# Kernel optimization log

Measured on AMD Instinct MI355X. Metric: run time of the kernel, lower is better.

Reference implementation:

```python
import jax, jax.numpy as jnp
import numpy as np

E = 8
DIMS = [512, 1024, 1024, 512]
BATCH = 2048


def _init_w(key, shape):
    a = np.sqrt(6.0 / (shape[-2] * shape[-1]))
    return jax.random.uniform(key, shape, dtype=jnp.float32, minval=-a, maxval=a)


def setup_inputs() -> dict:
    key = jax.random.key(0)
    ks = jax.random.split(key, 8)
    inp = {
        "weight_blend": jax.random.uniform(ks[0], (BATCH, E), dtype=jnp.float32),
        "x": jax.random.normal(ks[1], (BATCH, DIMS[0]), dtype=jnp.float32),
    }
    for i in range(3):
        inp[f"W{i}"] = _init_w(ks[2 + i], (E, DIMS[i + 1], DIMS[i]))
        inp[f"B{i}"] = jnp.zeros((E, DIMS[i + 1], 1), dtype=jnp.float32)
    return inp


def reference(weight_blend, x, W0, B0, W1, B1, W2, B2):
    Ws = [W0, W1, W2]
    Bs = [B0, B1, B2]
    acts = [jax.nn.elu, jax.nn.elu, None]
    for W, B, act in zip(Ws, Bs, acts):
        # dropout p=0 -> identity
        # blended-expert GEMM: sum_e wb[b,e] * (W[e] @ x[b]) == einsum
        t = jnp.einsum("be,eoi,bi->bo", weight_blend, W, x)
        bias = jnp.einsum("be,eo->bo", weight_blend, B[..., 0])
        x = t + bias
        if act is not None:
            x = act(x)
    return x
```

## Files before the change

### kernel.cpp

```cpp
#include <hip/hip_runtime.h>
#include <math.h>

typedef __attribute__((ext_vector_type(8))) short bf16x8;
typedef __attribute__((ext_vector_type(4))) float f32x4;

#define NEXP 8
#define BATCH 2048

__device__ __forceinline__ unsigned short f2bf(float f) {
    union { float f; unsigned u; } v; v.f = f;
    unsigned r = v.u + 0x7FFFu + ((v.u >> 16) & 1u);
    return (unsigned short)(r >> 16);
}

__device__ __forceinline__ float elu_fast(float v) {
    return v > 0.f ? v : (exp2f(v * 1.4426950408889634f) - 1.0f);
}

__global__ __launch_bounds__(256) void pack_all(
    const float* __restrict__ W0, const float* __restrict__ W1,
    const float* __restrict__ W2, const float* __restrict__ x,
    unsigned short* __restrict__ W0p, unsigned short* __restrict__ W1p,
    unsigned short* __restrict__ W2p, unsigned short* __restrict__ x0p)
{
    __shared__ float T[128 * 36];
    const int bid = blockIdx.x, t = threadIdx.x;

    if (bid < 10240) {
        const float* W; unsigned short* out; int KB, Din, Dout, U, lin;
        if (bid < 2048)      { W = W0; out = W0p; KB = 16; Din = 512;  Dout = 1024; U = 4; lin = bid; }
        else if (bid < 6144) { W = W1; out = W1p; KB = 32; Din = 1024; Dout = 1024; U = 4; lin = bid - 2048; }
        else                 { W = W2; out = W2p; KB = 32; Din = 1024; Dout = 512;  U = 2; lin = bid - 6144; }
        const int e  = lin & 7;
        const int r  = lin >> 3;
        const int kb = r % KB;
        const int nb = r / KB;
        const int N0 = nb * 16 * U;
        const int K0 = kb * 32;
        for (int it = 0; it < U / 2; ++it) {
            const int idx = t + 256 * it;
            const int nl = idx >> 3, k4 = (idx & 7) * 4;
            float4 v = *(const float4*)(W + ((size_t)e * Dout + N0 + nl) * Din + K0 + k4);
            *(float4*)(T + nl * 36 + k4) = v;
        }
        __syncthreads();
        if (t < 64 * U) {
            const int u = t >> 6, l = t & 63;
            const float* p = T + (u * 16 + (l & 15)) * 36 + (l >> 4) * 8;
            bf16x8 h;
            #pragma unroll
            for (int j = 0; j < 8; ++j) h[j] = (short)f2bf(p[j]);
            *(bf16x8*)(out + (size_t)lin * (U * 512) + t * 8) = h;
        }
    } else {
        const int lin = bid - 10240;
        const int kb = lin & 15, mb = lin >> 4;
        for (int it = 0; it < 4; ++it) {
            const int idx = t + 256 * it;
            const int ml = idx >> 3, k4 = (idx & 7) * 4;
            float4 v = *(const float4*)(x + (size_t)(mb * 128 + ml) * 512 + kb * 32 + k4);
            *(float4*)(T + ml * 36 + k4) = v;
        }
        __syncthreads();
        #pragma unroll
        for (int it = 0; it < 2; ++it) {
            const int s = t + 256 * it;
            const int g = s >> 6, l = s & 63;
            const float* p = T + (g * 16 + (l & 15)) * 36 + (l >> 4) * 8;
            bf16x8 h;
            #pragma unroll
            for (int j = 0; j < 8; ++j) h[j] = (short)f2bf(p[j]);
            *(bf16x8*)(x0p + (size_t)lin * 4096 + s * 8) = h;
        }
    }
}

template<int UP, int NU>
__device__ __forceinline__ void moe_body(
    float* lds_f, int bx, int by,
    const unsigned short* __restrict__ Xp,
    const unsigned short* __restrict__ Wp,
    const float* __restrict__ Bias,
    const float* __restrict__ WBl,
    void* __restrict__ Yout,
    int KB, int Dout, int KBn, int act, int packed_out)
{
    constexpr int PSTR = NU * 16 + 4;

    const int tid  = threadIdx.x;
    const int ew   = tid >> 6;
    const int l    = tid & 63;
    const int lh   = l >> 4;
    const int ll   = l & 15;
    const int e0   = 2 * ew;
    const int m0   = by * 64;
    const int n0   = bx * (NU * 16);
    const int mb   = by >> 1;
    const int half = by & 1;

    f32x4 acc0[4][NU], acc1[4][NU];
    #pragma unroll
    for (int t = 0; t < 4; ++t)
        #pragma unroll
        for (int u = 0; u < NU; ++u)
            #pragma unroll
            for (int i = 0; i < 4; ++i) { acc0[t][u][i] = 0.f; acc1[t][u][i] = 0.f; }

    unsigned aoff[4];
    #pragma unroll
    for (int t = 0; t < 4; ++t)
        aoff[t] = (unsigned)(mb * KB) * 8192u + (unsigned)(half * 4 + t) * 1024u + l * 16u;
    unsigned boff0[NU], boff1[NU];
    #pragma unroll
    for (int u = 0; u < NU; ++u) {
        const int fn = bx * NU + u;
        const int nb = fn / UP;
        const int uu = fn % UP;
        boff0[u] = (((unsigned)(nb * KB) * 8 + e0) * UP + uu) * 1024u + l * 16u;
        boff1[u] = boff0[u] + UP * 1024u;
    }
    const unsigned astr = 8192u;
    const unsigned bstr = UP * 8192u;
    const char* xc = (const char*)Xp;
    const char* wc = (const char*)Wp;

    bf16x8 aR[2][4], b0R[2][NU], b1R[2][NU];

    auto LOAD = [&](int s, int kk) {
        const unsigned ab = (unsigned)kk * astr;
        const unsigned bb = (unsigned)kk * bstr;
        #pragma unroll
        for (int t = 0; t < 4; ++t)
            aR[s][t] = *(const bf16x8*)(xc + aoff[t] + ab);
        #pragma unroll
        for (int u = 0; u < NU; ++u) {
            b0R[s][u] = *(const bf16x8*)(wc + boff0[u] + bb);
            b1R[s][u] = *(const bf16x8*)(wc + boff1[u] + bb);
        }
    };
    auto MF = [&](int s) {
        __builtin_amdgcn_s_setprio(1);
        #pragma unroll
        for (int u = 0; u < NU; ++u)
            #pragma unroll
            for (int t = 0; t < 4; ++t) {
                acc0[t][u] = __builtin_amdgcn_mfma_f32_16x16x32_bf16(aR[s][t], b0R[s][u], acc0[t][u], 0, 0, 0);
                acc1[t][u] = __builtin_amdgcn_mfma_f32_16x16x32_bf16(aR[s][t], b1R[s][u], acc1[t][u], 0, 0, 0);
            }
        __builtin_amdgcn_s_setprio(0);
    };

    LOAD(0, 0);
    for (int kk = 0; kk < KB; kk += 2) {
        if (kk + 1 < KB) LOAD(1, kk + 1);
        MF(0);
        if (kk + 2 < KB) LOAD(0, kk + 2);
        MF(1);
    }

    float bi0[NU], bi1[NU];
    #pragma unroll
    for (int u = 0; u < NU; ++u) {
        const int n = n0 + u * 16 + ll;
        bi0[u] = Bias[(size_t)e0 * Dout + n];
        bi1[u] = Bias[(size_t)(e0 + 1) * Dout + n];
    }
    float2 wbp[4][4];
    #pragma unroll
    for (int t = 0; t < 4; ++t)
        #pragma unroll
        for (int r = 0; r < 4; ++r) {
            const int lm = 16 * t + 4 * lh + r;
            wbp[t][r] = ((const float2*)(WBl + (size_t)(m0 + lm) * NEXP))[ew];
        }

    float* pb = lds_f + ew * (64 * PSTR);
    #pragma unroll
    for (int t = 0; t < 4; ++t)
        #pragma unroll
        for (int r = 0; r < 4; ++r) {
            const int lm = 16 * t + 4 * lh + r;
            #pragma unroll
            for (int u = 0; u < NU; ++u)
                pb[lm * PSTR + u * 16 + ll] =
                    wbp[t][r].x * (acc0[t][u][r] + bi0[u]) + wbp[t][r].y * (acc1[t][u][r] + bi1[u]);
        }
    __syncthreads();

    if (packed_out) {
        if constexpr (NU == 4) {
            #pragma unroll
            for (int it = 0; it < 2; ++it) {
                const int kbh = it;
                const int g   = tid >> 6;
                const int le  = tid & 63;
                const int lhh = le >> 4, lle = le & 15;
                const int rb  = (g * 16 + lle) * PSTR + kbh * 32 + lhh * 8;
                bf16x8 h;
                #pragma unroll
                for (int j = 0; j < 8; ++j) {
                    float v = lds_f[0 * 64 * PSTR + rb + j]
                            + lds_f[1 * 64 * PSTR + rb + j]
                            + lds_f[2 * 64 * PSTR + rb + j]
                            + lds_f[3 * 64 * PSTR + rb + j];
                    if (act) v = elu_fast(v);
                    h[j] = (short)f2bf(v);
                }
                unsigned short* dst = (unsigned short*)Yout +
                    ((size_t)(mb * KBn + bx * 2 + kbh) * 8 + half * 4 + g) * 512 + le * 8;
                *(bf16x8*)dst = h;
            }
        }
    } else {
        constexpr int F4R = NU * 4;
        #pragma unroll
        for (int it = 0; it < NU; ++it) {
            const int idx = tid + 256 * it;
            const int row = idx / F4R;
            const int c4  = (idx % F4R) * 4;
            const int rb  = row * PSTR + c4;
            float4 s  = *(const float4*)(lds_f + 0 * 64 * PSTR + rb);
            float4 q1 = *(const float4*)(lds_f + 1 * 64 * PSTR + rb);
            float4 q2 = *(const float4*)(lds_f + 2 * 64 * PSTR + rb);
            float4 q3 = *(const float4*)(lds_f + 3 * 64 * PSTR + rb);
            s.x += q1.x + q2.x + q3.x;
            s.y += q1.y + q2.y + q3.y;
            s.z += q1.z + q2.z + q3.z;
            s.w += q1.w + q2.w + q3.w;
            if (act) {
                s.x = elu_fast(s.x);
                s.y = elu_fast(s.y);
                s.z = elu_fast(s.z);
                s.w = elu_fast(s.w);
            }
            *(float4*)((float*)Yout + (size_t)(m0 + row) * Dout + n0 + c4) = s;
        }
    }
}

__device__ __forceinline__ void swz_pair(int& bx, int& by) {
    const int bid = blockIdx.x;
    const int xcd = bid & 7;
    const int loc = bid >> 3;
    bx = xcd * 2 + (loc & 1);
    by = loc >> 1;
}

__global__ __launch_bounds__(256, 2) void moe_l0(
    const unsigned short* __restrict__ Xp, const unsigned short* __restrict__ Wp,
    const float* __restrict__ Bias, const float* __restrict__ WBl,
    void* __restrict__ Yout, int KB, int Dout, int KBn, int act, int packed_out)
{
    __shared__ __align__(16) float lds_f[4 * 64 * 68];
    int bx, by; swz_pair(bx, by);
    moe_body<4, 4>(lds_f, bx, by, Xp, Wp, Bias, WBl, Yout, KB, Dout, KBn, act, packed_out);
}
__global__ __launch_bounds__(256, 2) void moe_l1(
    const unsigned short* __restrict__ Xp, const unsigned short* __restrict__ Wp,
    const float* __restrict__ Bias, const float* __restrict__ WBl,
    void* __restrict__ Yout, int KB, int Dout, int KBn, int act, int packed_out)
{
    __shared__ __align__(16) float lds_f[4 * 64 * 68];
    int bx, by; swz_pair(bx, by);
    moe_body<4, 4>(lds_f, bx, by, Xp, Wp, Bias, WBl, Yout, KB, Dout, KBn, act, packed_out);
}
__global__ __launch_bounds__(256, 2) void moe_l2(
    const unsigned short* __restrict__ Xp, const unsigned short* __restrict__ Wp,
    const float* __restrict__ Bias, const float* __restrict__ WBl,
    void* __restrict__ Yout, int KB, int Dout, int KBn, int act, int packed_out)
{
    __shared__ __align__(16) float lds_f[4 * 64 * 36];
    int bx, by; swz_pair(bx, by);
    moe_body<2, 2>(lds_f, bx, by, Xp, Wp, Bias, WBl, Yout, KB, Dout, KBn, act, packed_out);
}

#define BM 64
#define BNF 64
#define BKF 16
#define PAD 4

__global__ __launch_bounds__(256) void moe_layer_f32(
    const float* __restrict__ X, const float* __restrict__ W,
    const float* __restrict__ Bias, const float* __restrict__ WB,
    float* __restrict__ Y, int Din, int Dout, int act)
{
    __shared__ float As[BKF][BM + PAD];
    __shared__ float Bs[BKF][BNF + PAD];
    const int tid = threadIdx.x;
    const int tm = tid >> 4, tn = tid & 15;
    const int m0 = blockIdx.y * BM, n0 = blockIdx.x * BNF;
    const int lr = tid >> 2, lc = (tid & 3) << 2;
    float acc[4][4] = {};
    const float* xrow  = X  + (size_t)(m0 + lr) * Din;
    const float* wbrow = WB + (size_t)(m0 + lr) * NEXP;
    const float* wrow0 = W  + (size_t)(n0 + lr) * Din;
    for (int e = 0; e < NEXP; ++e) {
        const float wbe = wbrow[e];
        const float* wrow = wrow0 + (size_t)e * Dout * Din;
        for (int k0 = 0; k0 < Din; k0 += BKF) {
            float4 av = *(const float4*)(xrow + k0 + lc);
            float4 bv = *(const float4*)(wrow + k0 + lc);
            __syncthreads();
            As[lc+0][lr] = av.x*wbe; As[lc+1][lr] = av.y*wbe;
            As[lc+2][lr] = av.z*wbe; As[lc+3][lr] = av.w*wbe;
            Bs[lc+0][lr] = bv.x; Bs[lc+1][lr] = bv.y;
            Bs[lc+2][lr] = bv.z; Bs[lc+3][lr] = bv.w;
            __syncthreads();
            #pragma unroll
            for (int k = 0; k < BKF; ++k) {
                float4 a = *(const float4*)&As[k][tm << 2];
                float4 b = *(const float4*)&Bs[k][tn << 2];
                acc[0][0]+=a.x*b.x; acc[0][1]+=a.x*b.y; acc[0][2]+=a.x*b.z; acc[0][3]+=a.x*b.w;
                acc[1][0]+=a.y*b.x; acc[1][1]+=a.y*b.y; acc[1][2]+=a.y*b.z; acc[1][3]+=a.y*b.w;
                acc[2][0]+=a.z*b.x; acc[2][1]+=a.z*b.y; acc[2][2]+=a.z*b.z; acc[2][3]+=a.z*b.w;
                acc[3][0]+=a.w*b.x; acc[3][1]+=a.w*b.y; acc[3][2]+=a.w*b.z; acc[3][3]+=a.w*b.w;
            }
        }
    }
    #pragma unroll
    for (int im = 0; im < 4; ++im) {
        const int m = m0 + (tm << 2) + im;
        const float* wbm = WB + (size_t)m * NEXP;
        float wv[NEXP];
        #pragma unroll
        for (int e = 0; e < NEXP; ++e) wv[e] = wbm[e];
        #pragma unroll
        for (int in = 0; in < 4; ++in) {
            const int n = n0 + (tn << 2) + in;
            float bsum = 0.f;
            #pragma unroll
            for (int e = 0; e < NEXP; ++e) bsum += wv[e] * Bias[(size_t)e * Dout + n];
            float v = acc[im][in] + bsum;
            if (act) v = v > 0.f ? v : expm1f(v);
            acc[im][in] = v;
        }
        float4 o = make_float4(acc[im][0], acc[im][1], acc[im][2], acc[im][3]);
        *(float4*)(Y + (size_t)m * Dout + n0 + (tn << 2)) = o;
    }
}

extern "C" void kernel_launch(void* const* d_in, const int* in_sizes, int n_in,
                              void* d_out, int out_size, void* d_ws, size_t ws_size,
                              hipStream_t stream)
{
    (void)in_sizes; (void)n_in; (void)out_size;
    const float* wb = (const float*)d_in[0];
    const float* x  = (const float*)d_in[1];
    const float* W0 = (const float*)d_in[2];
    const float* B0 = (const float*)d_in[3];
    const float* W1 = (const float*)d_in[4];
    const float* B1 = (const float*)d_in[5];
    const float* W2 = (const float*)d_in[6];
    const float* B2 = (const float*)d_in[7];
    float* out = (float*)d_out;

    const size_t NW0 = (size_t)8*1024*512, NW1 = (size_t)8*1024*1024, NW2 = (size_t)8*512*1024;
    const size_t NX0 = (size_t)BATCH*512, NX1 = (size_t)BATCH*1024;
    const size_t need = (NW0 + NW1 + NW2 + NX0 + 2 * NX1) * 2;

    if (ws_size >= need) {
        unsigned short* W0p = (unsigned short*)d_ws;
        unsigned short* W1p = W0p + NW0;
        unsigned short* W2p = W1p + NW1;
        unsigned short* x0p = W2p + NW2;
        unsigned short* x1p = x0p + NX0;
        unsigned short* x2p = x1p + NX1;
        pack_all<<<10496, 256, 0, stream>>>(W0, W1, W2, x, W0p, W1p, W2p, x0p);
        moe_l0<<<512, 256, 0, stream>>>(x0p, W0p, B0, wb, x1p, 16, 1024, 32, 1, 1);
        moe_l1<<<512, 256, 0, stream>>>(x1p, W1p, B1, wb, x2p, 32, 1024, 32, 1, 1);
        moe_l2<<<512, 256, 0, stream>>>(x2p, W2p, B2, wb, out, 32, 512,  0, 0, 0);
    } else {
        float* x1 = (float*)d_ws;
        float* x2 = x1 + (size_t)BATCH * 1024;
        moe_layer_f32<<<dim3(1024/BNF, BATCH/BM), 256, 0, stream>>>(x,  W0, B0, wb, x1, 512,  1024, 1);
        moe_layer_f32<<<dim3(1024/BNF, BATCH/BM), 256, 0, stream>>>(x1, W1, B1, wb, x2, 1024, 1024, 1);
        moe_layer_f32<<<dim3(512/BNF,  BATCH/BM), 256, 0, stream>>>(x2, W2, B2, wb, out, 1024, 512,  0);
    }
}
```

Baseline: 191.6 us.

## Use 512-thread 128-row tiles with register double-buffered loads for layers 0-1

Adds a new MoE body for layers 0 and 1 where each 512-thread block covers 128 batch rows. Two row-halves of waves share the same weight fragments, which halves weight traffic per output. Global loads are double-buffered in registers ahead of the MFMAs, with wave priority raised during MFMA issue. The expert reduction through LDS is done in two passes over the row halves, adding an extra barrier. The grid halves to 256 blocks, so occupancy and load balance across CUs change, and the larger per-thread accumulator state raises register pressure.

```diff
diff --git a/kernel.cpp b/kernel.cpp
--- a/kernel.cpp
+++ b/kernel.cpp
@@ -72,6 +72,145 @@
             for (int j = 0; j < 8; ++j) h[j] = (short)f2bf(p[j]);
             *(bf16x8*)(x0p + (size_t)lin * 4096 + s * 8) = h;
         }
+    }
+}
+
+template<int UP>
+__device__ __forceinline__ void moe_body128(
+    float* lds_f, int bx, int by,
+    const unsigned short* __restrict__ Xp,
+    const unsigned short* __restrict__ Wp,
+    const float* __restrict__ Bias,
+    const float* __restrict__ WBl,
+    unsigned short* __restrict__ Yout,
+    int KB, int Dout, int KBn)
+{
+    constexpr int PSTR = 68;
+
+    const int tid  = threadIdx.x;
+    const int wv   = tid >> 6;
+    const int mh   = wv >> 2;
+    const int ew   = wv & 3;
+    const int l    = tid & 63;
+    const int lh   = l >> 4;
+    const int ll   = l & 15;
+    const int e0   = 2 * ew;
+    const int m0   = by * 128 + mh * 64;
+    const int n0   = bx * 64;
+    const int mb   = by;
+
+    f32x4 acc0[4][4], acc1[4][4];
+    #pragma unroll
+    for (int t = 0; t < 4; ++t)
+        #pragma unroll
+        for (int u = 0; u < 4; ++u)
+            #pragma unroll
+            for (int i = 0; i < 4; ++i) { acc0[t][u][i] = 0.f; acc1[t][u][i] = 0.f; }
+
+    unsigned aoff[4];
+    #pragma unroll
+    for (int t = 0; t < 4; ++t)
+        aoff[t] = (unsigned)(mb * KB) * 8192u + (unsigned)(mh * 4 + t) * 1024u + l * 16u;
+    unsigned boff0[4], boff1[4];
+    #pragma unroll
+    for (int u = 0; u < 4; ++u) {
+        const int fn = bx * 4 + u;
+        const int nb = fn / UP;
+        const int uu = fn % UP;
+        boff0[u] = (((unsigned)(nb * KB) * 8 + e0) * UP + uu) * 1024u + l * 16u;
+        boff1[u] = boff0[u] + UP * 1024u;
+    }
+    const unsigned astr = 8192u;
+    const unsigned bstr = UP * 8192u;
+    const char* xc = (const char*)Xp;
+    const char* wc = (const char*)Wp;
+
+    bf16x8 aR[2][4], b0R[2][4], b1R[2][4];
+
+    auto LOAD = [&](int s, int kk) {
+        const unsigned ab = (unsigned)kk * astr;
+        const unsigned bb = (unsigned)kk * bstr;
+        #pragma unroll
+        for (int t = 0; t < 4; ++t)
+            aR[s][t] = *(const bf16x8*)(xc + aoff[t] + ab);
+        #pragma unroll
+        for (int u = 0; u < 4; ++u) {
+            b0R[s][u] = *(const bf16x8*)(wc + boff0[u] + bb);
+            b1R[s][u] = *(const bf16x8*)(wc + boff1[u] + bb);
+        }
+    };
+    auto MF = [&](int s) {
+        __builtin_amdgcn_s_setprio(1);
+        #pragma unroll
+        for (int u = 0; u < 4; ++u)
+            #pragma unroll
+            for (int t = 0; t < 4; ++t) {
+                acc0[t][u] = __builtin_amdgcn_mfma_f32_16x16x32_bf16(aR[s][t], b0R[s][u], acc0[t][u], 0, 0, 0);
+                acc1[t][u] = __builtin_amdgcn_mfma_f32_16x16x32_bf16(aR[s][t], b1R[s][u], acc1[t][u], 0, 0, 0);
+            }
+        __builtin_amdgcn_s_setprio(0);
+    };
+
+    LOAD(0, 0);
+    for (int kk = 0; kk < KB; kk += 2) {
+        if (kk + 1 < KB) LOAD(1, kk + 1);
+        MF(0);
+        if (kk + 2 < KB) LOAD(0, kk + 2);
+        MF(1);
+    }
+
+    float bi0[4], bi1[4];
+    #pragma unroll
+    for (int u = 0; u < 4; ++u) {
+        const int n = n0 + u * 16 + ll;
+        bi0[u] = Bias[(size_t)e0 * Dout + n];
+        bi1[u] = Bias[(size_t)(e0 + 1) * Dout + n];
+    }
+    float2 wbp[4][4];
+    #pragma unroll
+    for (int t = 0; t < 4; ++t)
+        #pragma unroll
+        for (int r = 0; r < 4; ++r) {
+            const int lm = 16 * t + 4 * lh + r;
+            wbp[t][r] = ((const float2*)(WBl + (size_t)(m0 + lm) * NEXP))[ew];
+        }
+
+    float* pb = lds_f + ew * (64 * PSTR);
+
+    #pragma unroll
+    for (int h = 0; h < 2; ++h) {
+        if (mh == h) {
+            #pragma unroll
+            for (int t = 0; t < 4; ++t)
+                #pragma unroll
+                for (int r = 0; r < 4; ++r) {
+                    const int lm = 16 * t + 4 * lh + r;
+                    #pragma unroll
+                    for (int u = 0; u < 4; ++u)
+                        pb[lm * PSTR + u * 16 + ll] =
+                            wbp[t][r].x * (acc0[t][u][r] + bi0[u]) + wbp[t][r].y * (acc1[t][u][r] + bi1[u]);
+                }
+        }
+        __syncthreads();
+        {
+            const int kbh = wv >> 2;
+            const int g   = wv & 3;
+            const int rb  = (g * 16 + ll) * PSTR + kbh * 32 + lh * 8;
+            bf16x8 hx;
+            #pragma unroll
+            for (int j = 0; j < 8; ++j) {
+                float v = lds_f[0 * 64 * PSTR + rb + j]
+                        + lds_f[1 * 64 * PSTR + rb + j]
+                        + lds_f[2 * 64 * PSTR + rb + j]
+                        + lds_f[3 * 64 * PSTR + rb + j];
+                v = elu_fast(v);
+                hx[j] = (short)f2bf(v);
+            }
+            unsigned short* dst = Yout +
+                ((size_t)(mb * KBn + bx * 2 + kbh) * 8 + h * 4 + g) * 512 + l * 8;
+            *(bf16x8*)dst = hx;
+        }
+        if (h == 0) __syncthreads();
     }
 }
 
@@ -238,6 +377,13 @@
     }
 }
 
+__device__ __forceinline__ void swz256(int& bx, int& by) {
+    const int bid = blockIdx.x;
+    const int xcd = bid & 7;
+    const int loc = bid >> 3;
+    bx = xcd * 2 + (loc & 1);
+    by = loc >> 1;
+}
 __device__ __forceinline__ void swz_pair(int& bx, int& by) {
     const int bid = blockIdx.x;
     const int xcd = bid & 7;
@@ -246,23 +392,23 @@
     by = loc >> 1;
 }
 
-__global__ __launch_bounds__(256, 2) void moe_l0(
+__global__ __launch_bounds__(512, 2) void moe_l0(
     const unsigned short* __restrict__ Xp, const unsigned short* __restrict__ Wp,
     const float* __restrict__ Bias, const float* __restrict__ WBl,
-    void* __restrict__ Yout, int KB, int Dout, int KBn, int act, int packed_out)
+    unsigned short* __restrict__ Yout, int KB, int Dout, int KBn)
 {
     __shared__ __align__(16) float lds_f[4 * 64 * 68];
-    int bx, by; swz_pair(bx, by);
-    moe_body<4, 4>(lds_f, bx, by, Xp, Wp, Bias, WBl, Yout, KB, Dout, KBn, act, packed_out);
-}
-__global__ __launch_bounds__(256, 2) void moe_l1(
+    int bx, by; swz256(bx, by);
+    moe_body128<4>(lds_f, bx, by, Xp, Wp, Bias, WBl, Yout, KB, Dout, KBn);
+}
+__global__ __launch_bounds__(512, 2) void moe_l1(
     const unsigned short* __restrict__ Xp, const unsigned short* __restrict__ Wp,
     const float* __restrict__ Bias, const float* __restrict__ WBl,
-    void* __restrict__ Yout, int KB, int Dout, int KBn, int act, int packed_out)
+    unsigned short* __restrict__ Yout, int KB, int Dout, int KBn)
 {
     __shared__ __align__(16) float lds_f[4 * 64 * 68];
-    int bx, by; swz_pair(bx, by);
-    moe_body<4, 4>(lds_f, bx, by, Xp, Wp, Bias, WBl, Yout, KB, Dout, KBn, act, packed_out);
+    int bx, by; swz256(bx, by);
+    moe_body128<4>(lds_f, bx, by, Xp, Wp, Bias, WBl, Yout, KB, Dout, KBn);
 }
 __global__ __launch_bounds__(256, 2) void moe_l2(
     const unsigned short* __restrict__ Xp, const unsigned short* __restrict__ Wp,
@@ -366,8 +512,8 @@
         unsigned short* x1p = x0p + NX0;
         unsigned short* x2p = x1p + NX1;
         pack_all<<<10496, 256, 0, stream>>>(W0, W1, W2, x, W0p, W1p, W2p, x0p);
-        moe_l0<<<512, 256, 0, stream>>>(x0p, W0p, B0, wb, x1p, 16, 1024, 32, 1, 1);
-        moe_l1<<<512, 256, 0, stream>>>(x1p, W1p, B1, wb, x2p, 32, 1024, 32, 1, 1);
+        moe_l0<<<256, 512, 0, stream>>>(x0p, W0p, B0, wb, x1p, 16, 1024, 32);
+        moe_l1<<<256, 512, 0, stream>>>(x1p, W1p, B1, wb, x2p, 32, 1024, 32);
         moe_l2<<<512, 256, 0, stream>>>(x2p, W2p, B2, wb, out, 32, 512,  0, 0, 0);
     } else {
         float* x1 = (float*)d_ws;
```

New measurement: 192.3 us. About the same (+0.4%).
